# Kernel optimization log

Measured on AMD Instinct MI355X. Metric: run time of the kernel, lower is better.

## Reference

```python
import jax, jax.numpy as jnp
import numpy as np

N = 50000      # nodes
E = 800000     # edges
D_IN = 128     # raw feature dim
H = 96         # hidden_channels
K = 8          # experts
L = 4          # num_layers
C = 40         # classes


def setup_inputs() -> dict:
    key = jax.random.key(0)
    ks = jax.random.split(key, 10)
    stdv = 1.0 / np.sqrt(H)
    inp = {
        'x': jax.random.normal(ks[0], (N, D_IN), dtype=jnp.float32),
        'edge_index': jax.random.randint(ks[1], (2, E), 0, N, dtype=jnp.int64),
        # fcs[0]: Linear(d, hidden); fcs[1]: Linear(hidden, c)
        'fc0_w': jax.random.normal(ks[2], (D_IN, H), dtype=jnp.float32) * 0.05,
        'fc0_b': jnp.zeros((H,), dtype=jnp.float32),
        'fc1_w': jax.random.normal(ks[3], (H, C), dtype=jnp.float32) * 0.05,
        'fc1_b': jnp.zeros((C,), dtype=jnp.float32),
        # context_enc (method='node'): per-layer Linear(hidden, K)
        'ctx_w': jax.random.normal(ks[4], (L, H, K), dtype=jnp.float32) * 0.05,
        'ctx_b': jnp.zeros((L, K), dtype=jnp.float32),
        # GraphMultiConvolution weights: [L, K, hidden, hidden], uniform(-stdv, stdv)
        'conv_w': jax.random.uniform(ks[5], (L, K, H, H), dtype=jnp.float32,
                                     minval=-stdv, maxval=stdv),
    }
    return inp


def reference(x, edge_index, fc0_w, fc0_b, fc1_w, fc1_b, ctx_w, ctx_b, conv_w):
    # eval-mode forward (training=False): no dropout, softmax routing
    row = edge_index[0]
    col = edge_index[1]
    h = jax.nn.relu(x @ fc0_w + fc0_b)                     # [N, H]
    for i in range(L):
        # routing logits and soft expert weights z: [N, K]
        z = jax.nn.softmax(h @ ctx_w[i] + ctx_b[i], axis=-1)
        # spmm aggregation: hi[r] = sum over edges (r, c) of h[c]
        hi = jax.ops.segment_sum(h[col], row, num_segments=N)  # [N, H]
        # K-expert batched matmul: [N, K, H]
        outs = jnp.einsum('nd,kdo->nko', hi, conv_w[i])
        # gumbel/softmax-weighted combine + residual
        out = jnp.einsum('nk,nko->no', z, outs) + h
        h = jax.nn.relu(out)
    return h @ fc1_w + fc1_b                               # [N, C]
```

## Files before the change

### kernel.cpp

```cpp
#include <hip/hip_runtime.h>

#define N_NODES 50000
#define N_EDGES 800000
#define DIN     128
#define H       96
#define K_EXP   8
#define L_LAYERS 4
#define C_OUT   40

typedef _Float16 f16;
typedef f16 f16x2 __attribute__((ext_vector_type(2)));
typedef f16 f16x4 __attribute__((ext_vector_type(4)));
typedef f16 f16x8 __attribute__((ext_vector_type(8)));
typedef float f32x4 __attribute__((ext_vector_type(4)));


#define CONV_TOT (L_LAYERS * K_EXP * H * H)
#define FC0_TOT  (DIN * H)
#define FC1_TOT  (48 * H)
#define CNT_BLOCKS ((N_EDGES + 255) / 256)
#define CVT_BLOCKS ((CONV_TOT + FC0_TOT + FC1_TOT + 255) / 256)

__global__ __launch_bounds__(256) void count_convert(const int* __restrict__ row,
                                                     int* __restrict__ deg,
                                                     int* __restrict__ p,
                                                     const float* __restrict__ conv_w,
                                                     const float* __restrict__ fc0_w,
                                                     const float* __restrict__ fc1_w,
                                                     f16* __restrict__ wfrag,
                                                     f16* __restrict__ fc0t,
                                                     f16* __restrict__ fc1t) {
    int tid = threadIdx.x;
    if ((int)blockIdx.x < CNT_BLOCKS) {
        int i = blockIdx.x * 256 + tid;
        if (i < N_EDGES) p[i] = atomicAdd(&deg[row[i]], 1);
    } else {
        int i = ((int)blockIdx.x - CNT_BLOCKS) * 256 + tid;
        if (i < CONV_TOT) {
            int o = i % H;
            int t = i / H;
            int d = t % H;
            int lk = t / H;
            int ct = o >> 4, lc = o & 15;
            int ks = d >> 5, quad = (d >> 3) & 3, j = d & 7;
            wfrag[(size_t)lk * 9216 + ct * 1536 + ks * 512 + (quad * 16 + lc) * 8 + j] =
                (f16)conv_w[i];
        } else if (i < CONV_TOT + FC0_TOT) {
            int j = i - CONV_TOT;
            int o = j % H, d = j / H;
            fc0t[o * DIN + d] = (f16)fc0_w[j];
        } else if (i < CONV_TOT + FC0_TOT + FC1_TOT) {
            int j = i - CONV_TOT - FC0_TOT;
            int o = j / H, d = j % H;
            fc1t[j] = (o < C_OUT) ? (f16)fc1_w[d * C_OUT + o] : (f16)0.f;
        }
    }
}

__global__ __launch_bounds__(1024) void scanA(const int* __restrict__ deg,
                                              int* __restrict__ rowptr,
                                              int* __restrict__ partial, int n) {
    __shared__ int wsum[16];
    int tid  = threadIdx.x;
    int lane = tid & 63, wid = tid >> 6;
    int idx = blockIdx.x * 1024 + tid;
    int v = (idx < n) ? deg[idx] : 0;
    int s = v;
    #pragma unroll
    for (int off = 1; off < 64; off <<= 1) {
        int t = __shfl_up(s, off, 64);
        if (lane >= off) s += t;
    }
    if (lane == 63) wsum[wid] = s;
    __syncthreads();
    if (wid == 0 && lane < 16) {
        int w = wsum[lane];
        #pragma unroll
        for (int off = 1; off < 16; off <<= 1) {
            int t = __shfl_up(w, off, 16);
            if (lane >= off) w += t;
        }
        wsum[lane] = w;
    }
    __syncthreads();
    int waveoff = (wid == 0) ? 0 : wsum[wid - 1];
    if (idx < n) rowptr[idx + 1] = waveoff + s;
    if (tid == 1023) partial[blockIdx.x] = waveoff + s;
}

__global__ __launch_bounds__(1024) void scanC(int* __restrict__ rowptr,
                                              const int* __restrict__ partial,
                                              int nb, int n) {
    __shared__ int boff_s;
    int tid = threadIdx.x;
    if (tid < 64) {
        int v = 0;
        for (int j = tid; j < (int)blockIdx.x; j += 64) v += partial[j];
        #pragma unroll
        for (int off = 32; off >= 1; off >>= 1) v += __shfl_xor(v, off, 64);
        if (tid == 0) boff_s = v;
    }
    __syncthreads();
    int boff = boff_s;
    int idx = blockIdx.x * 1024 + tid;
    if (idx == 0) rowptr[0] = 0;
    if (idx < n) rowptr[idx + 1] += boff;
}


#define SCT_BLOCKS 1024
#define FPAD 136

__global__ __launch_bounds__(256) void scatter_fc0(const int* __restrict__ row,
                                                   const int* __restrict__ col,
                                                   const int* __restrict__ p,
                                                   const int* __restrict__ rowptr,
                                                   int* __restrict__ csr,
                                                   const float* __restrict__ x,
                                                   const f16* __restrict__ fc0t,
                                                   const float* __restrict__ b,
                                                   f16* __restrict__ h16, int n) {
    __shared__ f16 As[64 * FPAD];
    __shared__ f16 Ws[96 * FPAD];
    int tid = threadIdx.x;
    if ((int)blockIdx.x < SCT_BLOCKS) {
        int stride = SCT_BLOCKS * 256;
        for (int i = blockIdx.x * 256 + tid; i < N_EDGES; i += stride)
            csr[rowptr[row[i]] + p[i]] = col[i];
        return;
    }
    int l = tid & 63, w = tid >> 6;
    int quad = l >> 4, lc = l & 15;
    int row0 = ((int)blockIdx.x - SCT_BLOCKS) * 64;

    for (int t = tid; t < 2048; t += 256) {
        int m = t >> 5, c4 = (t & 31) * 4;
        int gr = row0 + m;
        float4 v = {0.f, 0.f, 0.f, 0.f};
        if (gr < n) v = *(const float4*)(x + (size_t)gr * DIN + c4);
        f16x4 h4 = {(f16)v.x, (f16)v.y, (f16)v.z, (f16)v.w};
        *(f16x4*)&As[m * FPAD + c4] = h4;
    }
    for (int t = tid; t < 1536; t += 256) {
        int o = t >> 4, c8 = (t & 15) * 8;
        *(f16x8*)&Ws[o * FPAD + c8] = *(const f16x8*)(fc0t + o * DIN + c8);
    }
    __syncthreads();

    f16x8 afr[4];
    #pragma unroll
    for (int ks = 0; ks < 4; ks++)
        afr[ks] = *(const f16x8*)&As[(16 * w + lc) * FPAD + ks * 32 + quad * 8];

    f32x4 acc[6] = {};
    #pragma unroll
    for (int ct = 0; ct < 6; ct++) {
        #pragma unroll
        for (int ks = 0; ks < 4; ks++) {
            f16x8 bfr = *(const f16x8*)&Ws[(ct * 16 + lc) * FPAD + ks * 32 + quad * 8];
            acc[ct] = __builtin_amdgcn_mfma_f32_16x16x32_f16(afr[ks], bfr, acc[ct], 0, 0, 0);
        }
    }

    int m0 = 16 * w + quad * 4;
    #pragma unroll
    for (int r = 0; r < 4; r++) {
        int gr = row0 + m0 + r;
        if (gr < n) {
            #pragma unroll
            for (int ct = 0; ct < 6; ct++) {
                int o = ct * 16 + lc;
                h16[(size_t)gr * H + o] = (f16)fmaxf(acc[ct][r] + b[o], 0.f);
            }
        }
    }
}


#define SPMM_BLOCKS ((N_NODES + 15) / 16)
#define CTX_BLOCKS  ((N_NODES + 255) / 256)

#define ACC8(v) { _Pragma("unroll") for (int q = 0; q < 8; q++) acc[q] += (float)(v)[q]; }

__global__ __launch_bounds__(256) void layer_pre(const f16* __restrict__ h16,
                                                 const int* __restrict__ rowptr,
                                                 const int* __restrict__ csr,
                                                 f16* __restrict__ hi16,
                                                 const float* __restrict__ cw,
                                                 const float* __restrict__ cb,
                                                 float* __restrict__ zt, int n) {
    __shared__ float ws[H * K_EXP];
    __shared__ float bs[K_EXP];
    int tid = threadIdx.x;
    if ((int)blockIdx.x < SPMM_BLOCKS) {
        int r  = blockIdx.x * 16 + (tid >> 4);
        int li = tid & 15;
        if (r >= n) return;
        bool act = li < 12;
        int j = rowptr[r], e = rowptr[r + 1];
        float acc[8] = {};
        const f16* hb = h16 + li * 8;

        int4 qa = *(const int4*)(csr + j);
        int4 qb = *(const int4*)(csr + j + 4);

        while (j + 8 <= e) {
            int4 na = *(const int4*)(csr + j + 8);
            int4 nb = *(const int4*)(csr + j + 12);
            f16x8 v0 = {}, v1 = {}, v2 = {}, v3 = {}, v4 = {}, v5 = {}, v6 = {}, v7 = {};
            if (act) {
                v0 = *(const f16x8*)(hb + (size_t)qa.x * H);
                v1 = *(const f16x8*)(hb + (size_t)qa.y * H);
                v2 = *(const f16x8*)(hb + (size_t)qa.z * H);
                v3 = *(const f16x8*)(hb + (size_t)qa.w * H);
                v4 = *(const f16x8*)(hb + (size_t)qb.x * H);
                v5 = *(const f16x8*)(hb + (size_t)qb.y * H);
                v6 = *(const f16x8*)(hb + (size_t)qb.z * H);
                v7 = *(const f16x8*)(hb + (size_t)qb.w * H);
            }
            ACC8(v0) ACC8(v1) ACC8(v2) ACC8(v3)
            ACC8(v4) ACC8(v5) ACC8(v6) ACC8(v7)
            j += 8; qa = na; qb = nb;
        }
        if (j + 4 <= e) {
            f16x8 v0 = {}, v1 = {}, v2 = {}, v3 = {};
            if (act) {
                v0 = *(const f16x8*)(hb + (size_t)qa.x * H);
                v1 = *(const f16x8*)(hb + (size_t)qa.y * H);
                v2 = *(const f16x8*)(hb + (size_t)qa.z * H);
                v3 = *(const f16x8*)(hb + (size_t)qa.w * H);
            }
            ACC8(v0) ACC8(v1) ACC8(v2) ACC8(v3)
            j += 4; qa = qb;
        }
        int rem = e - j;
        if (rem > 0) {
            f16x8 v0 = {}, v1 = {}, v2 = {};
            if (act) {
                v0 = *(const f16x8*)(hb + (size_t)qa.x * H);
                if (rem > 1) v1 = *(const f16x8*)(hb + (size_t)qa.y * H);
                if (rem > 2) v2 = *(const f16x8*)(hb + (size_t)qa.z * H);
            }
            ACC8(v0)
            if (rem > 1) ACC8(v1)
            if (rem > 2) ACC8(v2)
        }
        if (act) {
            f16x8 o;
            #pragma unroll
            for (int q = 0; q < 8; q++) o[q] = (f16)acc[q];
            *(f16x8*)(hi16 + (size_t)r * H + li * 8) = o;
        }
    } else {
        for (int t = tid; t < H * K_EXP; t += 256) ws[t] = cw[t];
        if (tid < K_EXP) bs[tid] = cb[tid];
        __syncthreads();
        int node = ((int)blockIdx.x - SPMM_BLOCKS) * 256 + tid;
        if (node >= n) return;
        float acc[K_EXP];
        #pragma unroll
        for (int k = 0; k < K_EXP; k++) acc[k] = bs[k];
        const f16* hr = h16 + (size_t)node * H;
        #pragma unroll 3
        for (int c8 = 0; c8 < 12; c8++) {
            f16x8 v = *(const f16x8*)(hr + c8 * 8);
            #pragma unroll
            for (int j = 0; j < 8; j++) {
                float hv = (float)v[j];
                int d = c8 * 8 + j;
                #pragma unroll
                for (int k = 0; k < K_EXP; k++) acc[k] += hv * ws[d * K_EXP + k];
            }
        }
        float mx = acc[0];
        #pragma unroll
        for (int k = 1; k < K_EXP; k++) mx = fmaxf(mx, acc[k]);
        float s = 0.f;
        #pragma unroll
        for (int k = 0; k < K_EXP; k++) { acc[k] = __expf(acc[k] - mx); s += acc[k]; }
        float inv = 1.f / s;
        f32x4 za = {acc[0] * inv, acc[1] * inv, acc[2] * inv, acc[3] * inv};
        f32x4 zb = {acc[4] * inv, acc[5] * inv, acc[6] * inv, acc[7] * inv};
        *(f32x4*)(zt + (size_t)node * K_EXP) = za;
        *(f32x4*)(zt + (size_t)node * K_EXP + 4) = zb;
    }
}


#define EG_STAGE 2
#define EG_HALFS (EG_STAGE * 9216)

__global__ __launch_bounds__(256) void expert_gemm(const f16* __restrict__ hi16,
                                                   const f16* __restrict__ hin16,
                                                   const f16* __restrict__ wfrag,
                                                   const float* __restrict__ zt,
                                                   f16* __restrict__ hout16, int n) {
    __shared__ f16 Wl[EG_HALFS];
    int tid = threadIdx.x;
    int l = tid & 63, w = tid >> 6;
    int quad = l >> 4, lc = l & 15;
    int brow = blockIdx.x * 128;
    int wrow0 = brow + w * 16;
    int wrow1 = wrow0 + 64;

    f16x8 afr0[3], afr1[3];
    #pragma unroll
    for (int ks = 0; ks < 3; ks++) {
        afr0[ks] = *(const f16x8*)(hi16 + (size_t)(wrow0 + lc) * H + ks * 32 + quad * 8);
        afr1[ks] = *(const f16x8*)(hi16 + (size_t)(wrow1 + lc) * H + ks * 32 + quad * 8);
    }

    f32x4 z0a = *(const f32x4*)(zt + (size_t)(wrow0 + lc) * K_EXP);
    f32x4 z0b = *(const f32x4*)(zt + (size_t)(wrow0 + lc) * K_EXP + 4);
    f32x4 z1a = *(const f32x4*)(zt + (size_t)(wrow1 + lc) * K_EXP);
    f32x4 z1b = *(const f32x4*)(zt + (size_t)(wrow1 + lc) * K_EXP + 4);
    f16 zh0[K_EXP], zh1[K_EXP];
    #pragma unroll
    for (int k = 0; k < 4; k++) {
        zh0[k] = (f16)z0a[k]; zh0[k + 4] = (f16)z0b[k];
        zh1[k] = (f16)z1a[k]; zh1[k + 4] = (f16)z1b[k];
    }

    f32x4 acc0[6] = {};
    f32x4 acc1[6] = {};

    for (int kb = 0; kb < K_EXP; kb += EG_STAGE) {
        __syncthreads();
        const f16* src = wfrag + (size_t)kb * 9216;
        for (int t = tid; t < EG_HALFS / 8; t += 256)
            *(f16x8*)&Wl[t * 8] = *(const f16x8*)(src + t * 8);
        __syncthreads();

        #pragma unroll
        for (int k2 = 0; k2 < EG_STAGE; k2++) {
            int k = kb + k2;
            f16 s0 = zh0[k], s1 = zh1[k];
            f16x8 a0s[3], a1s[3];
            #pragma unroll
            for (int ks = 0; ks < 3; ks++) {
                a0s[ks] = afr0[ks] * s0;
                a1s[ks] = afr1[ks] * s1;
            }
            #pragma unroll
            for (int ct = 0; ct < 6; ct++) {
                f16x8 b0 = *(const f16x8*)&Wl[k2 * 9216 + ct * 1536 + 0 * 512 + l * 8];
                f16x8 b1 = *(const f16x8*)&Wl[k2 * 9216 + ct * 1536 + 1 * 512 + l * 8];
                f16x8 b2 = *(const f16x8*)&Wl[k2 * 9216 + ct * 1536 + 2 * 512 + l * 8];
                acc0[ct] = __builtin_amdgcn_mfma_f32_16x16x32_f16(a0s[0], b0, acc0[ct], 0, 0, 0);
                acc0[ct] = __builtin_amdgcn_mfma_f32_16x16x32_f16(a0s[1], b1, acc0[ct], 0, 0, 0);
                acc0[ct] = __builtin_amdgcn_mfma_f32_16x16x32_f16(a0s[2], b2, acc0[ct], 0, 0, 0);
                acc1[ct] = __builtin_amdgcn_mfma_f32_16x16x32_f16(a1s[0], b0, acc1[ct], 0, 0, 0);
                acc1[ct] = __builtin_amdgcn_mfma_f32_16x16x32_f16(a1s[1], b1, acc1[ct], 0, 0, 0);
                acc1[ct] = __builtin_amdgcn_mfma_f32_16x16x32_f16(a1s[2], b2, acc1[ct], 0, 0, 0);
            }
        }
    }

    #pragma unroll
    for (int r = 0; r < 4; r++) {
        int gr0 = wrow0 + quad * 4 + r;
        if (gr0 < n) {
            #pragma unroll
            for (int ct = 0; ct < 6; ct++) {
                int o = ct * 16 + lc;
                float v = fmaxf(acc0[ct][r] + (float)hin16[(size_t)gr0 * H + o], 0.f);
                hout16[(size_t)gr0 * H + o] = (f16)v;
            }
        }
        int gr1 = wrow1 + quad * 4 + r;
        if (gr1 < n) {
            #pragma unroll
            for (int ct = 0; ct < 6; ct++) {
                int o = ct * 16 + lc;
                float v = fmaxf(acc1[ct][r] + (float)hin16[(size_t)gr1 * H + o], 0.f);
                hout16[(size_t)gr1 * H + o] = (f16)v;
            }
        }
    }
}


#define APAD 104

__global__ __launch_bounds__(256) void fc1_kernel(const f16* __restrict__ h16,
                                                  const f16* __restrict__ fc1t,
                                                  const float* __restrict__ b,
                                                  float* __restrict__ out, int n) {
    __shared__ f16 As[64 * APAD];
    __shared__ f16 Ws[48 * APAD];
    int tid = threadIdx.x;
    int l = tid & 63, w = tid >> 6;
    int quad = l >> 4, lc = l & 15;
    int row0 = blockIdx.x * 64;

    for (int t = tid; t < 768; t += 256) {
        int m = t / 12, c8 = (t % 12) * 8;
        int gr = row0 + m;
        f16x8 v = {};
        if (gr < n) v = *(const f16x8*)(h16 + (size_t)gr * H + c8);
        *(f16x8*)&As[m * APAD + c8] = v;
    }
    for (int t = tid; t < 576; t += 256) {
        int o = t / 12, c8 = (t % 12) * 8;
        *(f16x8*)&Ws[o * APAD + c8] = *(const f16x8*)(fc1t + o * H + c8);
    }
    __syncthreads();

    f16x8 afr[3];
    #pragma unroll
    for (int ks = 0; ks < 3; ks++)
        afr[ks] = *(const f16x8*)&As[(16 * w + lc) * APAD + ks * 32 + quad * 8];

    f32x4 acc[3] = {};
    #pragma unroll
    for (int ct = 0; ct < 3; ct++) {
        #pragma unroll
        for (int ks = 0; ks < 3; ks++) {
            f16x8 bfr = *(const f16x8*)&Ws[(ct * 16 + lc) * APAD + ks * 32 + quad * 8];
            acc[ct] = __builtin_amdgcn_mfma_f32_16x16x32_f16(afr[ks], bfr, acc[ct], 0, 0, 0);
        }
    }

    int m0 = 16 * w + quad * 4;
    #pragma unroll
    for (int r = 0; r < 4; r++) {
        int gr = row0 + m0 + r;
        if (gr < n) {
            #pragma unroll
            for (int ct = 0; ct < 3; ct++) {
                int o = ct * 16 + lc;
                if (o < C_OUT)
                    out[(size_t)gr * C_OUT + o] = acc[ct][r] + b[o];
            }
        }
    }
}


extern "C" void kernel_launch(void* const* d_in, const int* in_sizes, int n_in,
                              void* d_out, int out_size, void* d_ws, size_t ws_size,
                              hipStream_t stream) {
    const float* x      = (const float*)d_in[0];
    const int*   ei     = (const int*)d_in[1];
    const float* fc0_w  = (const float*)d_in[2];
    const float* fc0_b  = (const float*)d_in[3];
    const float* fc1_w  = (const float*)d_in[4];
    const float* fc1_b  = (const float*)d_in[5];
    const float* ctx_w  = (const float*)d_in[6];
    const float* ctx_b  = (const float*)d_in[7];
    const float* conv_w = (const float*)d_in[8];
    float* out = (float*)d_out;

    const size_t NH = (size_t)N_NODES * H;

    float* zbuf = (float*)d_ws;
    f16*   h16a = (f16*)(zbuf + (size_t)N_NODES * K_EXP);
    f16*   h16b = h16a + NH;
    f16*   hi16 = h16b + NH;
    f16*   wfrag= hi16 + NH;
    f16*   fc0t = wfrag + CONV_TOT;
    f16*   fc1t = fc0t + FC0_TOT;
    int* rowptr = (int*)(fc1t + FC1_TOT);
    int* deg    = rowptr + (N_NODES + 1);
    int* csr    = deg + N_NODES;
    int* prank  = csr + N_EDGES;
    int* partial  = prank + N_EDGES;

    const int* row = ei;
    const int* col = ei + N_EDGES;

    hipMemsetAsync(deg, 0, sizeof(int) * N_NODES, stream);

    count_convert<<<CNT_BLOCKS + CVT_BLOCKS, 256, 0, stream>>>(
        row, deg, prank, conv_w, fc0_w, fc1_w, wfrag, fc0t, fc1t);
    int nsb = (N_NODES + 1023) / 1024;
    scanA<<<nsb, 1024, 0, stream>>>(deg, rowptr, partial, N_NODES);
    scanC<<<nsb, 1024, 0, stream>>>(rowptr, partial, nsb, N_NODES);

    int gemm_grid = (N_NODES + 63) / 64;
    scatter_fc0<<<SCT_BLOCKS + gemm_grid, 256, 0, stream>>>(
        row, col, prank, rowptr, csr, x, fc0t, fc0_b, h16a, N_NODES);

    int eg_grid = (N_NODES + 127) / 128;
    f16* hcur = h16a;
    f16* hnext = h16b;
    for (int i = 0; i < L_LAYERS; i++) {
        layer_pre<<<SPMM_BLOCKS + CTX_BLOCKS, 256, 0, stream>>>(
            hcur, rowptr, csr, hi16,
            ctx_w + (size_t)i * H * K_EXP, ctx_b + (size_t)i * K_EXP, zbuf, N_NODES);
        expert_gemm<<<eg_grid, 256, 0, stream>>>(
            hi16, hcur, wfrag + (size_t)i * K_EXP * H * H, zbuf, hnext, N_NODES);
        f16* t = hcur; hcur = hnext; hnext = t;
    }
    fc1_kernel<<<gemm_grid, 256, 0, stream>>>(hcur, fc1t, fc1_b, out, N_NODES);
}
```

Measured before the change: 350.6 us.

## Fuse SpMM aggregation, routing softmax and expert GEMM into one per-layer kernel

Replaces the two per-layer kernels with one layer_fused kernel. Each 64-row block gathers neighbor sums into LDS, computes the softmax routing weights for its rows into LDS, then runs the z-scaled MFMA expert GEMM straight from LDS. This removes the global round trip of the hi and z buffers and one launch per layer. In exchange, each block reloads all 8 expert weight tiles for only 64 rows, which is half the reuse of before. Only 64 of 256 threads do the context softmax, and all 256 wait at barriers between the phases.

```diff
diff --git a/kernel.cpp b/kernel.cpp
--- a/kernel.cpp
+++ b/kernel.cpp
@@ -177,203 +177,165 @@
 }
 
 
-#define SPMM_BLOCKS ((N_NODES + 15) / 16)
-#define CTX_BLOCKS  ((N_NODES + 255) / 256)
+#define LF_ROWS   64
+#define LF_BLOCKS ((N_NODES + LF_ROWS - 1) / LF_ROWS)
+#define HPAD      104
 
 #define ACC8(v) { _Pragma("unroll") for (int q = 0; q < 8; q++) acc[q] += (float)(v)[q]; }
 
-__global__ __launch_bounds__(256) void layer_pre(const f16* __restrict__ h16,
-                                                 const int* __restrict__ rowptr,
-                                                 const int* __restrict__ csr,
-                                                 f16* __restrict__ hi16,
-                                                 const float* __restrict__ cw,
-                                                 const float* __restrict__ cb,
-                                                 float* __restrict__ zt, int n) {
+__global__ __launch_bounds__(256, 4) void layer_fused(const f16* __restrict__ h16,
+                                                      const int* __restrict__ rowptr,
+                                                      const int* __restrict__ csr,
+                                                      const float* __restrict__ cw,
+                                                      const float* __restrict__ cb,
+                                                      const f16* __restrict__ wfrag,
+                                                      f16* __restrict__ hout16, int n) {
+    __shared__ f16 hi_lds[LF_ROWS * HPAD];
+    __shared__ f16 Wl[9216];
     __shared__ float ws[H * K_EXP];
+    __shared__ f16 z_lds[LF_ROWS * K_EXP];
     __shared__ float bs[K_EXP];
+
     int tid = threadIdx.x;
-    if ((int)blockIdx.x < SPMM_BLOCKS) {
-        int r  = blockIdx.x * 16 + (tid >> 4);
-        int li = tid & 15;
-        if (r >= n) return;
+    int brow = blockIdx.x * LF_ROWS;
+
+    for (int t = tid; t < H * K_EXP; t += 256) ws[t] = cw[t];
+    if (tid < K_EXP) bs[tid] = cb[tid];
+
+    {
+        int g = tid >> 4, li = tid & 15;
         bool act = li < 12;
-        int j = rowptr[r], e = rowptr[r + 1];
-        float acc[8] = {};
         const f16* hb = h16 + li * 8;
-
-        int4 qa = *(const int4*)(csr + j);
-        int4 qb = *(const int4*)(csr + j + 4);
-
-        while (j + 8 <= e) {
-            int4 na = *(const int4*)(csr + j + 8);
-            int4 nb = *(const int4*)(csr + j + 12);
-            f16x8 v0 = {}, v1 = {}, v2 = {}, v3 = {}, v4 = {}, v5 = {}, v6 = {}, v7 = {};
+        for (int sub = 0; sub < 4; sub++) {
+            int r = brow + g * 4 + sub;
+            if (r >= n) break;
+            int j = rowptr[r], e = rowptr[r + 1];
+            float acc[8] = {};
+            int4 qa = *(const int4*)(csr + j);
+            int4 qb = *(const int4*)(csr + j + 4);
+            while (j + 8 <= e) {
+                int4 na = *(const int4*)(csr + j + 8);
+                int4 nb = *(const int4*)(csr + j + 12);
+                f16x8 v0 = {}, v1 = {}, v2 = {}, v3 = {}, v4 = {}, v5 = {}, v6 = {}, v7 = {};
+                if (act) {
+                    v0 = *(const f16x8*)(hb + (size_t)qa.x * H);
+                    v1 = *(const f16x8*)(hb + (size_t)qa.y * H);
+                    v2 = *(const f16x8*)(hb + (size_t)qa.z * H);
+                    v3 = *(const f16x8*)(hb + (size_t)qa.w * H);
+                    v4 = *(const f16x8*)(hb + (size_t)qb.x * H);
+                    v5 = *(const f16x8*)(hb + (size_t)qb.y * H);
+                    v6 = *(const f16x8*)(hb + (size_t)qb.z * H);
+                    v7 = *(const f16x8*)(hb + (size_t)qb.w * H);
+                }
+                ACC8(v0) ACC8(v1) ACC8(v2) ACC8(v3)
+                ACC8(v4) ACC8(v5) ACC8(v6) ACC8(v7)
+                j += 8; qa = na; qb = nb;
+            }
+            if (j + 4 <= e) {
+                f16x8 v0 = {}, v1 = {}, v2 = {}, v3 = {};
+                if (act) {
+                    v0 = *(const f16x8*)(hb + (size_t)qa.x * H);
+                    v1 = *(const f16x8*)(hb + (size_t)qa.y * H);
+                    v2 = *(const f16x8*)(hb + (size_t)qa.z * H);
+                    v3 = *(const f16x8*)(hb + (size_t)qa.w * H);
+                }
+                ACC8(v0) ACC8(v1) ACC8(v2) ACC8(v3)
+                j += 4; qa = qb;
+            }
+            int rem = e - j;
+            if (rem > 0) {
+                f16x8 v0 = {}, v1 = {}, v2 = {};
+                if (act) {
+                    v0 = *(const f16x8*)(hb + (size_t)qa.x * H);
+                    if (rem > 1) v1 = *(const f16x8*)(hb + (size_t)qa.y * H);
+                    if (rem > 2) v2 = *(const f16x8*)(hb + (size_t)qa.z * H);
+                }
+                ACC8(v0)
+                if (rem > 1) ACC8(v1)
+                if (rem > 2) ACC8(v2)
+            }
             if (act) {
-                v0 = *(const f16x8*)(hb + (size_t)qa.x * H);
-                v1 = *(const f16x8*)(hb + (size_t)qa.y * H);
-                v2 = *(const f16x8*)(hb + (size_t)qa.z * H);
-                v3 = *(const f16x8*)(hb + (size_t)qa.w * H);
-                v4 = *(const f16x8*)(hb + (size_t)qb.x * H);
-                v5 = *(const f16x8*)(hb + (size_t)qb.y * H);
-                v6 = *(const f16x8*)(hb + (size_t)qb.z * H);
-                v7 = *(const f16x8*)(hb + (size_t)qb.w * H);
-            }
-            ACC8(v0) ACC8(v1) ACC8(v2) ACC8(v3)
-            ACC8(v4) ACC8(v5) ACC8(v6) ACC8(v7)
-            j += 8; qa = na; qb = nb;
-        }
-        if (j + 4 <= e) {
-            f16x8 v0 = {}, v1 = {}, v2 = {}, v3 = {};
-            if (act) {
-                v0 = *(const f16x8*)(hb + (size_t)qa.x * H);
-                v1 = *(const f16x8*)(hb + (size_t)qa.y * H);
-                v2 = *(const f16x8*)(hb + (size_t)qa.z * H);
-                v3 = *(const f16x8*)(hb + (size_t)qa.w * H);
-            }
-            ACC8(v0) ACC8(v1) ACC8(v2) ACC8(v3)
-            j += 4; qa = qb;
-        }
-        int rem = e - j;
-        if (rem > 0) {
-            f16x8 v0 = {}, v1 = {}, v2 = {};
-            if (act) {
-                v0 = *(const f16x8*)(hb + (size_t)qa.x * H);
-                if (rem > 1) v1 = *(const f16x8*)(hb + (size_t)qa.y * H);
-                if (rem > 2) v2 = *(const f16x8*)(hb + (size_t)qa.z * H);
-            }
-            ACC8(v0)
-            if (rem > 1) ACC8(v1)
-            if (rem > 2) ACC8(v2)
-        }
-        if (act) {
-            f16x8 o;
-            #pragma unroll
-            for (int q = 0; q < 8; q++) o[q] = (f16)acc[q];
-            *(f16x8*)(hi16 + (size_t)r * H + li * 8) = o;
-        }
-    } else {
-        for (int t = tid; t < H * K_EXP; t += 256) ws[t] = cw[t];
-        if (tid < K_EXP) bs[tid] = cb[tid];
-        __syncthreads();
-        int node = ((int)blockIdx.x - SPMM_BLOCKS) * 256 + tid;
-        if (node >= n) return;
-        float acc[K_EXP];
-        #pragma unroll
-        for (int k = 0; k < K_EXP; k++) acc[k] = bs[k];
-        const f16* hr = h16 + (size_t)node * H;
-        #pragma unroll 3
-        for (int c8 = 0; c8 < 12; c8++) {
-            f16x8 v = *(const f16x8*)(hr + c8 * 8);
-            #pragma unroll
-            for (int j = 0; j < 8; j++) {
-                float hv = (float)v[j];
-                int d = c8 * 8 + j;
+                f16x8 o;
                 #pragma unroll
-                for (int k = 0; k < K_EXP; k++) acc[k] += hv * ws[d * K_EXP + k];
-            }
-        }
-        float mx = acc[0];
-        #pragma unroll
-        for (int k = 1; k < K_EXP; k++) mx = fmaxf(mx, acc[k]);
-        float s = 0.f;
-        #pragma unroll
-        for (int k = 0; k < K_EXP; k++) { acc[k] = __expf(acc[k] - mx); s += acc[k]; }
-        float inv = 1.f / s;
-        f32x4 za = {acc[0] * inv, acc[1] * inv, acc[2] * inv, acc[3] * inv};
-        f32x4 zb = {acc[4] * inv, acc[5] * inv, acc[6] * inv, acc[7] * inv};
-        *(f32x4*)(zt + (size_t)node * K_EXP) = za;
-        *(f32x4*)(zt + (size_t)node * K_EXP + 4) = zb;
-    }
-}
-
-
-#define EG_STAGE 2
-#define EG_HALFS (EG_STAGE * 9216)
-
-__global__ __launch_bounds__(256) void expert_gemm(const f16* __restrict__ hi16,
-                                                   const f16* __restrict__ hin16,
-                                                   const f16* __restrict__ wfrag,
-                                                   const float* __restrict__ zt,
-                                                   f16* __restrict__ hout16, int n) {
-    __shared__ f16 Wl[EG_HALFS];
-    int tid = threadIdx.x;
+                for (int q = 0; q < 8; q++) o[q] = (f16)acc[q];
+                *(f16x8*)&hi_lds[(g * 4 + sub) * HPAD + li * 8] = o;
+            }
+        }
+    }
+
+    __syncthreads();
+    if (tid < LF_ROWS) {
+        int node = brow + tid;
+        if (node < n) {
+            float acc[K_EXP];
+            #pragma unroll
+            for (int k = 0; k < K_EXP; k++) acc[k] = bs[k];
+            const f16* hr = h16 + (size_t)node * H;
+            #pragma unroll 3
+            for (int c8 = 0; c8 < 12; c8++) {
+                f16x8 v = *(const f16x8*)(hr + c8 * 8);
+                #pragma unroll
+                for (int j = 0; j < 8; j++) {
+                    float hv = (float)v[j];
+                    int d = c8 * 8 + j;
+                    #pragma unroll
+                    for (int k = 0; k < K_EXP; k++) acc[k] += hv * ws[d * K_EXP + k];
+                }
+            }
+            float mx = acc[0];
+            #pragma unroll
+            for (int k = 1; k < K_EXP; k++) mx = fmaxf(mx, acc[k]);
+            float s = 0.f;
+            #pragma unroll
+            for (int k = 0; k < K_EXP; k++) { acc[k] = __expf(acc[k] - mx); s += acc[k]; }
+            float inv = 1.f / s;
+            f16x8 zo;
+            #pragma unroll
+            for (int k = 0; k < K_EXP; k++) zo[k] = (f16)(acc[k] * inv);
+            *(f16x8*)&z_lds[tid * K_EXP] = zo;
+        }
+    }
+    __syncthreads();
+
     int l = tid & 63, w = tid >> 6;
     int quad = l >> 4, lc = l & 15;
-    int brow = blockIdx.x * 128;
-    int wrow0 = brow + w * 16;
-    int wrow1 = wrow0 + 64;
-
-    f16x8 afr0[3], afr1[3];
-    #pragma unroll
-    for (int ks = 0; ks < 3; ks++) {
-        afr0[ks] = *(const f16x8*)(hi16 + (size_t)(wrow0 + lc) * H + ks * 32 + quad * 8);
-        afr1[ks] = *(const f16x8*)(hi16 + (size_t)(wrow1 + lc) * H + ks * 32 + quad * 8);
-    }
-
-    f32x4 z0a = *(const f32x4*)(zt + (size_t)(wrow0 + lc) * K_EXP);
-    f32x4 z0b = *(const f32x4*)(zt + (size_t)(wrow0 + lc) * K_EXP + 4);
-    f32x4 z1a = *(const f32x4*)(zt + (size_t)(wrow1 + lc) * K_EXP);
-    f32x4 z1b = *(const f32x4*)(zt + (size_t)(wrow1 + lc) * K_EXP + 4);
-    f16 zh0[K_EXP], zh1[K_EXP];
-    #pragma unroll
-    for (int k = 0; k < 4; k++) {
-        zh0[k] = (f16)z0a[k]; zh0[k + 4] = (f16)z0b[k];
-        zh1[k] = (f16)z1a[k]; zh1[k + 4] = (f16)z1b[k];
-    }
-
-    f32x4 acc0[6] = {};
-    f32x4 acc1[6] = {};
-
-    for (int kb = 0; kb < K_EXP; kb += EG_STAGE) {
-        __syncthreads();
-        const f16* src = wfrag + (size_t)kb * 9216;
-        for (int t = tid; t < EG_HALFS / 8; t += 256)
+
+    f16x8 afr[3];
+    #pragma unroll
+    for (int ks = 0; ks < 3; ks++)
+        afr[ks] = *(const f16x8*)&hi_lds[(w * 16 + lc) * HPAD + ks * 32 + quad * 8];
+    f16x8 zh = *(const f16x8*)&z_lds[(w * 16 + lc) * K_EXP];
+
+    f32x4 acc[6] = {};
+    for (int k = 0; k < K_EXP; k++) {
+        if (k) __syncthreads();
+        const f16* src = wfrag + (size_t)k * 9216;
+        for (int t = tid; t < 1152; t += 256)
             *(f16x8*)&Wl[t * 8] = *(const f16x8*)(src + t * 8);
         __syncthreads();
 
+        f16 s = zh[k];
+        f16x8 as0 = afr[0] * s, as1 = afr[1] * s, as2 = afr[2] * s;
         #pragma unroll
-        for (int k2 = 0; k2 < EG_STAGE; k2++) {
-            int k = kb + k2;
-            f16 s0 = zh0[k], s1 = zh1[k];
-            f16x8 a0s[3], a1s[3];
-            #pragma unroll
-            for (int ks = 0; ks < 3; ks++) {
-                a0s[ks] = afr0[ks] * s0;
-                a1s[ks] = afr1[ks] * s1;
-            }
-            #pragma unroll
-            for (int ct = 0; ct < 6; ct++) {
-                f16x8 b0 = *(const f16x8*)&Wl[k2 * 9216 + ct * 1536 + 0 * 512 + l * 8];
-                f16x8 b1 = *(const f16x8*)&Wl[k2 * 9216 + ct * 1536 + 1 * 512 + l * 8];
-                f16x8 b2 = *(const f16x8*)&Wl[k2 * 9216 + ct * 1536 + 2 * 512 + l * 8];
-                acc0[ct] = __builtin_amdgcn_mfma_f32_16x16x32_f16(a0s[0], b0, acc0[ct], 0, 0, 0);
-                acc0[ct] = __builtin_amdgcn_mfma_f32_16x16x32_f16(a0s[1], b1, acc0[ct], 0, 0, 0);
-                acc0[ct] = __builtin_amdgcn_mfma_f32_16x16x32_f16(a0s[2], b2, acc0[ct], 0, 0, 0);
-                acc1[ct] = __builtin_amdgcn_mfma_f32_16x16x32_f16(a1s[0], b0, acc1[ct], 0, 0, 0);
-                acc1[ct] = __builtin_amdgcn_mfma_f32_16x16x32_f16(a1s[1], b1, acc1[ct], 0, 0, 0);
-                acc1[ct] = __builtin_amdgcn_mfma_f32_16x16x32_f16(a1s[2], b2, acc1[ct], 0, 0, 0);
-            }
+        for (int ct = 0; ct < 6; ct++) {
+            f16x8 b0 = *(const f16x8*)&Wl[ct * 1536 + 0 * 512 + l * 8];
+            f16x8 b1 = *(const f16x8*)&Wl[ct * 1536 + 1 * 512 + l * 8];
+            f16x8 b2 = *(const f16x8*)&Wl[ct * 1536 + 2 * 512 + l * 8];
+            acc[ct] = __builtin_amdgcn_mfma_f32_16x16x32_f16(as0, b0, acc[ct], 0, 0, 0);
+            acc[ct] = __builtin_amdgcn_mfma_f32_16x16x32_f16(as1, b1, acc[ct], 0, 0, 0);
+            acc[ct] = __builtin_amdgcn_mfma_f32_16x16x32_f16(as2, b2, acc[ct], 0, 0, 0);
         }
     }
 
     #pragma unroll
     for (int r = 0; r < 4; r++) {
-        int gr0 = wrow0 + quad * 4 + r;
-        if (gr0 < n) {
+        int gr = brow + w * 16 + quad * 4 + r;
+        if (gr < n) {
             #pragma unroll
             for (int ct = 0; ct < 6; ct++) {
                 int o = ct * 16 + lc;
-                float v = fmaxf(acc0[ct][r] + (float)hin16[(size_t)gr0 * H + o], 0.f);
-                hout16[(size_t)gr0 * H + o] = (f16)v;
-            }
-        }
-        int gr1 = wrow1 + quad * 4 + r;
-        if (gr1 < n) {
-            #pragma unroll
-            for (int ct = 0; ct < 6; ct++) {
-                int o = ct * 16 + lc;
-                float v = fmaxf(acc1[ct][r] + (float)hin16[(size_t)gr1 * H + o], 0.f);
-                hout16[(size_t)gr1 * H + o] = (f16)v;
+                float v = fmaxf(acc[ct][r] + (float)h16[(size_t)gr * H + o], 0.f);
+                hout16[(size_t)gr * H + o] = (f16)v;
             }
         }
     }
@@ -453,11 +415,9 @@
 
     const size_t NH = (size_t)N_NODES * H;
 
-    float* zbuf = (float*)d_ws;
-    f16*   h16a = (f16*)(zbuf + (size_t)N_NODES * K_EXP);
+    f16*   h16a = (f16*)d_ws;
     f16*   h16b = h16a + NH;
-    f16*   hi16 = h16b + NH;
-    f16*   wfrag= hi16 + NH;
+    f16*   wfrag= h16b + NH;
     f16*   fc0t = wfrag + CONV_TOT;
     f16*   fc1t = fc0t + FC0_TOT;
     int* rowptr = (int*)(fc1t + FC1_TOT);
@@ -481,15 +441,13 @@
     scatter_fc0<<<SCT_BLOCKS + gemm_grid, 256, 0, stream>>>(
         row, col, prank, rowptr, csr, x, fc0t, fc0_b, h16a, N_NODES);
 
-    int eg_grid = (N_NODES + 127) / 128;
     f16* hcur = h16a;
     f16* hnext = h16b;
     for (int i = 0; i < L_LAYERS; i++) {
-        layer_pre<<<SPMM_BLOCKS + CTX_BLOCKS, 256, 0, stream>>>(
-            hcur, rowptr, csr, hi16,
-            ctx_w + (size_t)i * H * K_EXP, ctx_b + (size_t)i * K_EXP, zbuf, N_NODES);
-        expert_gemm<<<eg_grid, 256, 0, stream>>>(
-            hi16, hcur, wfrag + (size_t)i * K_EXP * H * H, zbuf, hnext, N_NODES);
+        layer_fused<<<LF_BLOCKS, 256, 0, stream>>>(
+            hcur, rowptr, csr,
+            ctx_w + (size_t)i * H * K_EXP, ctx_b + (size_t)i * K_EXP,
+            wfrag + (size_t)i * K_EXP * H * H, hnext, N_NODES);
         f16* t = hcur; hcur = hnext; hnext = t;
     }
     fc1_kernel<<<gemm_grid, 256, 0, stream>>>(hcur, fc1t, fc1_b, out, N_NODES);
```

Result: faster. 336.8 us (-4.0%).
